# Optimization experiments

Measured on AMD Instinct MI355X. Metric: run time of the kernel, lower is better.

The kernel has to match this reference:

```python
import jax, jax.numpy as jnp
import numpy as np

SHAPES = [(64, 64), (32, 32), (16, 16), (8, 8)]  # (H,W) per level, strides 8..64 of a 512px image
D, NH, NLV, NP, NLAYERS, DFF = 256, 8, 4, 4, 6, 1024
HD = D // NH
B = 4


def setup_inputs() -> dict:
    key = jax.random.key(0)
    ks = jax.random.split(key, 32)
    inp = {}
    for l, (h, w) in enumerate(SHAPES):
        inp[f"src{l}"] = jax.random.normal(ks[l], (B, D, h, w), jnp.float32)
        inp[f"pos{l}"] = jax.random.normal(ks[4 + l], (B, D, h, w), jnp.float32)
    s = 0.02
    p = lambda k, shape: jax.random.normal(k, shape, jnp.float32) * s
    inp["level_embed"] = p(ks[8], (NLV, D))
    inp["W_so"] = p(ks[9], (NLAYERS, D, NH * NLV * NP * 2)); inp["b_so"] = p(ks[10], (NLAYERS, NH * NLV * NP * 2))
    inp["W_aw"] = p(ks[11], (NLAYERS, D, NH * NLV * NP)); inp["b_aw"] = p(ks[12], (NLAYERS, NH * NLV * NP))
    inp["W_v"] = p(ks[13], (NLAYERS, D, D)); inp["b_v"] = p(ks[14], (NLAYERS, D))
    inp["W_o"] = p(ks[15], (NLAYERS, D, D)); inp["b_o"] = p(ks[16], (NLAYERS, D))
    inp["g1"] = jnp.ones((NLAYERS, D)); inp["be1"] = jnp.zeros((NLAYERS, D))
    inp["W_f1"] = p(ks[17], (NLAYERS, D, DFF)); inp["b_f1"] = p(ks[18], (NLAYERS, DFF))
    inp["W_f2"] = p(ks[19], (NLAYERS, DFF, D)); inp["b_f2"] = p(ks[20], (NLAYERS, D))
    inp["g2"] = jnp.ones((NLAYERS, D)); inp["be2"] = jnp.zeros((NLAYERS, D))
    return inp


def _layernorm(x, g, b):
    m = x.mean(-1, keepdims=True)
    v = x.var(-1, keepdims=True)
    return (x - m) * jax.lax.rsqrt(v + 1e-5) * g + b


def _reference_points():
    refs = []
    for (H_, W_) in SHAPES:
        ry = (jnp.arange(H_, dtype=jnp.float32) + 0.5) / H_
        rx = (jnp.arange(W_, dtype=jnp.float32) + 0.5) / W_
        gy, gx = jnp.meshgrid(ry, rx, indexing="ij")
        refs.append(jnp.stack([gx.ravel(), gy.ravel()], -1))
    return jnp.concatenate(refs, 0)  # [S,2] (x,y); valid_ratios==1 so same per level


def _ms_deform_sample(value, loc, aw):
    # value [B,S,NH,HD]; loc [B,S,NH,NLV,NP,2] (x,y in [0,1]); aw [B,S,NH,NLV,NP]
    Bq, S = value.shape[:2]
    v = value.transpose(0, 2, 1, 3)  # [B,NH,S,HD]
    out = jnp.zeros((Bq, NH, S, HD), value.dtype)
    start = 0
    for l, (H_, W_) in enumerate(SHAPES):
        n = H_ * W_
        vl = v[:, :, start:start + n, :]  # [B,NH,H_*W_,HD]
        start += n
        # grid_sample(align_corners=False) semantics: pixel = loc*size - 0.5, zero padding
        x = loc[:, :, :, l, :, 0] * W_ - 0.5  # [B,S,NH,NP]
        y = loc[:, :, :, l, :, 1] * H_ - 0.5
        x0 = jnp.floor(x); y0 = jnp.floor(y)
        wx1 = x - x0; wy1 = y - y0
        acc = jnp.zeros((Bq, NH, S * NP, HD), value.dtype)
        corners = ((0, 0, (1 - wx1) * (1 - wy1)), (1, 0, wx1 * (1 - wy1)),
                   (0, 1, (1 - wx1) * wy1), (1, 1, wx1 * wy1))
        for dx, dy, wgt in corners:
            xi = x0 + dx; yi = y0 + dy
            valid = (xi >= 0) & (xi < W_) & (yi >= 0) & (yi < H_)
            idx = (jnp.clip(yi, 0, H_ - 1) * W_ + jnp.clip(xi, 0, W_ - 1)).astype(jnp.int32)
            idx = idx.transpose(0, 2, 1, 3).reshape(Bq, NH, S * NP)
            w = (wgt * valid).transpose(0, 2, 1, 3).reshape(Bq, NH, S * NP)
            g = jnp.take_along_axis(vl, idx[..., None], axis=2)  # [B,NH,S*NP,HD]
            acc = acc + w[..., None] * g
        acc = acc.reshape(Bq, NH, S, NP, HD)
        awl = aw[:, :, :, l, :].transpose(0, 2, 1, 3)  # [B,NH,S,NP]
        out = out + (acc * awl[..., None]).sum(3)
    return out.transpose(0, 2, 1, 3).reshape(Bq, S, D)


def reference(src0, src1, src2, src3, pos0, pos1, pos2, pos3, level_embed,
              W_so, b_so, W_aw, b_aw, W_v, b_v, W_o, b_o, g1, be1,
              W_f1, b_f1, W_f2, b_f2, g2, be2):
    srcs = [src0, src1, src2, src3]
    poss = [pos0, pos1, pos2, pos3]
    src_flat, pos_flat = [], []
    for l in range(NLV):
        src_flat.append(srcs[l].reshape(B, D, -1).transpose(0, 2, 1))
        pos_flat.append(poss[l].reshape(B, D, -1).transpose(0, 2, 1) + level_embed[l])
    src = jnp.concatenate(src_flat, 1)   # [B,S,D]
    pos = jnp.concatenate(pos_flat, 1)
    S = src.shape[1]
    ref = _reference_points()  # [S,2]
    normalizer = jnp.array([[w, h] for (h, w) in SHAPES], jnp.float32)  # [NLV,2] = (W,H)

    out = src
    for i in range(NLAYERS):
        q = out + pos
        off = (q @ W_so[i] + b_so[i]).reshape(B, S, NH, NLV, NP, 2)
        loc = ref[None, :, None, None, None, :] + off / normalizer[None, None, None, :, None, :]
        aw = jax.nn.softmax((q @ W_aw[i] + b_aw[i]).reshape(B, S, NH, NLV * NP), -1)
        aw = aw.reshape(B, S, NH, NLV, NP)
        val = (out @ W_v[i] + b_v[i]).reshape(B, S, NH, HD)
        att = _ms_deform_sample(val, loc, aw) @ W_o[i] + b_o[i]
        x = _layernorm(out + att, g1[i], be1[i])
        ffn = jax.nn.relu(x @ W_f1[i] + b_f1[i]) @ W_f2[i] + b_f2[i]
        out = _layernorm(x + ffn, g2[i], be2[i])

    spatial_shapes = jnp.array(SHAPES, jnp.int32)
    level_start_index = jnp.concatenate([jnp.zeros((1,), jnp.int32),
                                         jnp.cumsum(spatial_shapes.prod(1))[:-1]])
    return out, spatial_shapes, level_start_index
```

## Files before the change

### kernel.cpp

```cpp
#include <hip/hip_runtime.h>
#include <cstdint>

#define SSn 5440
#define TTn 21760
#define TD ((size_t)TTn*256)
#define NL 6

typedef short bf16x8 __attribute__((ext_vector_type(8)));
typedef float f32x4 __attribute__((ext_vector_type(4)));
typedef float f32x2 __attribute__((ext_vector_type(2)));
typedef unsigned short u16x4 __attribute__((ext_vector_type(4)));
typedef unsigned short ushort_t;

__device__ __forceinline__ ushort_t f2b(float f) {
  uint32_t x = __float_as_uint(f);
  uint32_t r = x + 0x7FFFu + ((x >> 16) & 1u);
  return (ushort_t)(r >> 16);
}
__device__ __forceinline__ float b2f(ushort_t u) {
  return __uint_as_float((uint32_t)u << 16);
}

__global__ __launch_bounds__(256) void prep_kernel(
    const float* __restrict__ s0, const float* __restrict__ p0,
    const float* __restrict__ s1, const float* __restrict__ p1,
    const float* __restrict__ s2, const float* __restrict__ p2,
    const float* __restrict__ s3, const float* __restrict__ p3,
    const float* __restrict__ lev,
    float* __restrict__ cur, ushort_t* __restrict__ cur_b,
    ushort_t* __restrict__ pos_b, ushort_t* __restrict__ q_b)
{
  __shared__ float ts[64][65];
  __shared__ float tp[64][65];
  int bx = blockIdx.x;
  int b = bx / 340, r = bx % 340;
  const float *sp, *pp; int l, HW, start, dt, ptile;
  if (r < 256)      { l=0; HW=4096; start=0;    sp=s0; pp=p0; dt=r>>6;       ptile=r&63; }
  else if (r < 320) { l=1; HW=1024; start=4096; sp=s1; pp=p1; dt=(r-256)>>4; ptile=(r-256)&15; }
  else if (r < 336) { l=2; HW=256;  start=5120; sp=s2; pp=p2; dt=(r-320)>>2; ptile=(r-320)&3; }
  else              { l=3; HW=64;   start=5376; sp=s3; pp=p3; dt=r-336;      ptile=0; }
  int d0 = dt * 64, pp0 = ptile * 64;
  int t = threadIdx.x;
  int rr = t >> 2, c4 = (t & 3) * 16;
  size_t ibase = ((size_t)b * 256 + d0 + rr) * HW + pp0;
  #pragma unroll
  for (int i = 0; i < 4; ++i) {
    f32x4 v = *(const f32x4*)(sp + ibase + c4 + i * 4);
    f32x4 w = *(const f32x4*)(pp + ibase + c4 + i * 4);
    #pragma unroll
    for (int j = 0; j < 4; ++j) { ts[c4 + i*4 + j][rr] = v[j]; tp[c4 + i*4 + j][rr] = w[j]; }
  }
  __syncthreads();
  int token = start + pp0 + rr;
  size_t obase = ((size_t)b * SSn + token) * 256 + d0;
  #pragma unroll
  for (int i = 0; i < 4; ++i) {
    f32x4 cv; u16x4 cb, pb, qb;
    #pragma unroll
    for (int j = 0; j < 4; ++j) {
      float c = ts[rr][c4 + i*4 + j];
      float p = tp[rr][c4 + i*4 + j] + lev[l * 256 + d0 + c4 + i*4 + j];
      cv[j] = c; cb[j] = f2b(c); pb[j] = f2b(p); qb[j] = f2b(c + p);
    }
    *(f32x4*)(cur + obase + c4 + i*4) = cv;
    *(u16x4*)(cur_b + obase + c4 + i*4) = cb;
    *(u16x4*)(pos_b + obase + c4 + i*4) = pb;
    *(u16x4*)(q_b + obase + c4 + i*4) = qb;
  }
}

__global__ __launch_bounds__(256) void wprep_kernel(
    const float* __restrict__ W_so, const float* __restrict__ W_aw,
    const float* __restrict__ W_v,  const float* __restrict__ W_o,
    const float* __restrict__ W_f1, const float* __restrict__ W_f2,
    ushort_t* __restrict__ wt)
{
  __shared__ float tile[64][65];
  int bx = blockIdx.x;
  int layer = bx / 184, r = bx % 184;
  int type, ti;
  if (r < 16)       { type = 0; ti = r; }
  else if (r < 24)  { type = 1; ti = r - 16; }
  else if (r < 40)  { type = 2; ti = r - 24; }
  else if (r < 56)  { type = 3; ti = r - 40; }
  else if (r < 120) { type = 4; ti = r - 56; }
  else              { type = 5; ti = r - 120; }
  const float* src;
  int K, N, dof;
  switch (type) {
    case 0: src = W_so + (size_t)layer * 65536;  K = 256;  N = 256;  dof = 0;      break;
    case 1: src = W_aw + (size_t)layer * 32768;  K = 256;  N = 128;  dof = 65536;  break;
    case 2: src = W_v  + (size_t)layer * 65536;  K = 256;  N = 256;  dof = 98304;  break;
    case 3: src = W_o  + (size_t)layer * 65536;  K = 256;  N = 256;  dof = 163840; break;
    case 4: src = W_f1 + (size_t)layer * 262144; K = 256;  N = 1024; dof = 229376; break;
    default:src = W_f2 + (size_t)layer * 262144; K = 1024; N = 256;  dof = 491520; break;
  }
  int Kt = K >> 6;
  int k0 = (ti % Kt) * 64, n0 = (ti / Kt) * 64;
  ushort_t* dst = wt + (size_t)layer * 753664 + dof;
  int t = threadIdx.x;
  int rr = t >> 2, c4 = (t & 3) * 16;
  #pragma unroll
  for (int i = 0; i < 4; ++i) {
    f32x4 v = *(const f32x4*)(src + (size_t)(k0 + rr) * N + n0 + c4 + i * 4);
    tile[c4 + i*4 + 0][rr] = v[0];
    tile[c4 + i*4 + 1][rr] = v[1];
    tile[c4 + i*4 + 2][rr] = v[2];
    tile[c4 + i*4 + 3][rr] = v[3];
  }
  __syncthreads();
  int vrow = ((rr & 3) << 4) | (rr >> 2);
  #pragma unroll
  for (int i = 0; i < 4; ++i) {
    u16x4 o;
    #pragma unroll
    for (int j = 0; j < 4; ++j) o[j] = f2b(tile[rr][c4 + i*4 + j]);
    *(u16x4*)(dst + (size_t)(n0 + vrow) * K + k0 + c4 + i * 4) = o;
  }
}

__global__ void bias_fuse(const float* __restrict__ bso,
                          const float* __restrict__ baw,
                          float* __restrict__ bsa)
{
  int l = blockIdx.x, t = threadIdx.x;
  bsa[l * 384 + t] = (t < 256) ? bso[l * 256 + t] : baw[l * 128 + t - 256];
}

__device__ __forceinline__ void gemm_body8(
    ushort_t* As, ushort_t* Bs,
    const ushort_t* __restrict__ A, const ushort_t* __restrict__ Bt,
    const float* __restrict__ bias, ushort_t* __restrict__ Cb,
    int N, int n0, int m0, int K, int relu)
{
  int t = threadIdx.x;
  int l = t & 63, w = t >> 6;
  int wr = w >> 1, wc = w & 1;
  int lq = l >> 4, l15 = l & 15, r7 = l & 7;
  f32x4 acc[4][4] = {};

  for (int k0 = 0; k0 < K; k0 += 64) {
    #pragma unroll
    for (int i = 0; i < 4; ++i) {
      int c = i * 512 + t;
      int row = c >> 3;
      int sc = (c & 7) ^ (row & 7);
      __builtin_amdgcn_global_load_lds(
          (const uint32_t*)(A + (size_t)(m0 + row) * K + k0 + sc * 8),
          (uint32_t*)((char*)As + c * 16), 16, 0, 0);
    }
    #pragma unroll
    for (int i = 0; i < 2; ++i) {
      int c = i * 512 + t;
      int row = c >> 3;
      int sc = (c & 7) ^ (row & 7);
      __builtin_amdgcn_global_load_lds(
          (const uint32_t*)(Bt + (size_t)(n0 + row) * K + k0 + sc * 8),
          (uint32_t*)((char*)Bs + c * 16), 16, 0, 0);
    }
    __syncthreads();
    #pragma unroll
    for (int ks = 0; ks < 2; ++ks) {
      bf16x8 af[4], bfr[4];
      int chs = ((ks << 2) + lq) ^ r7;
      #pragma unroll
      for (int mt = 0; mt < 4; ++mt)
        af[mt] = *(const bf16x8*)((const char*)As +
                   (wr * 64 + mt * 16 + l15) * 128 + (chs << 4));
      #pragma unroll
      for (int nt = 0; nt < 4; ++nt)
        bfr[nt] = *(const bf16x8*)((const char*)Bs +
                   (wc * 64 + nt * 16 + l15) * 128 + (chs << 4));
      #pragma unroll
      for (int mt = 0; mt < 4; ++mt)
        #pragma unroll
        for (int nt = 0; nt < 4; ++nt)
          acc[mt][nt] = __builtin_amdgcn_mfma_f32_16x16x32_bf16(
              af[mt], bfr[nt], acc[mt][nt], 0, 0, 0);
    }
    __syncthreads();
  }

  int crow0 = m0 + wr * 64;
  int cb = n0 + wc * 64 + l15 * 4;
  f32x4 bv4 = *(const f32x4*)(bias + cb);
  #pragma unroll
  for (int mt = 0; mt < 4; ++mt) {
    #pragma unroll
    for (int r = 0; r < 4; ++r) {
      int rowg = crow0 + mt * 16 + lq * 4 + r;
      u16x4 o;
      #pragma unroll
      for (int nt = 0; nt < 4; ++nt) {
        float v = acc[mt][nt][r] + bv4[nt];
        if (relu) v = fmaxf(v, 0.f);
        o[nt] = f2b(v);
      }
      *(u16x4*)(Cb + (size_t)rowg * N + cb) = o;
    }
  }
}

__global__ __launch_bounds__(512) void gemm_mfma(
    const ushort_t* __restrict__ A, const ushort_t* __restrict__ Bt,
    const float* __restrict__ bias, ushort_t* __restrict__ Cb,
    int N, int K, int relu)
{
  __shared__ alignas(16) ushort_t As[16384];
  __shared__ alignas(16) ushort_t Bs[8192];
  gemm_body8(As, Bs, A, Bt, bias, Cb, N, blockIdx.y * 128, blockIdx.x * 256, K, relu);
}

__global__ __launch_bounds__(512) void gemm_dual(
    const ushort_t* __restrict__ A0, const ushort_t* __restrict__ Bt0,
    const float* __restrict__ bias0, ushort_t* __restrict__ C0,
    const ushort_t* __restrict__ A1, const ushort_t* __restrict__ Bt1,
    const float* __restrict__ bias1, ushort_t* __restrict__ C1,
    int K)
{
  __shared__ alignas(16) ushort_t As[16384];
  __shared__ alignas(16) ushort_t Bs[8192];
  int gy = blockIdx.y;
  if (gy < 3)
    gemm_body8(As, Bs, A0, Bt0, bias0, C0, 384, gy * 128, blockIdx.x * 256, K, 0);
  else
    gemm_body8(As, Bs, A1, Bt1, bias1, C1, 256, (gy - 3) * 128, blockIdx.x * 256, K, 0);
}

__global__ __launch_bounds__(512) void gemm_ln(
    const ushort_t* __restrict__ A, const ushort_t* __restrict__ Bt,
    const float* __restrict__ bias, const float* __restrict__ res,
    const float* __restrict__ g, const float* __restrict__ be,
    float* __restrict__ Of, ushort_t* __restrict__ Ob,
    ushort_t* __restrict__ Oq, const ushort_t* __restrict__ posb,
    int K)
{
  __shared__ alignas(16) ushort_t As[64 * 64];
  __shared__ alignas(16) ushort_t Bs[256 * 64];
  __shared__ float psum[64][4];
  __shared__ float psum2[64][4];
  __shared__ float2 mstd[64];
  int t = threadIdx.x;
  int l = t & 63, w = t >> 6;
  int wr = w >> 2, wc = w & 3;
  int m0 = blockIdx.x * 64;
  int lq = l >> 4, l15 = l & 15, r7 = l & 7;
  f32x4 acc[2][4] = {};

  for (int k0 = 0; k0 < K; k0 += 64) {
    {
      int c = t;
      int row = c >> 3;
      int sc = (c & 7) ^ (row & 7);
      __builtin_amdgcn_global_load_lds(
          (const uint32_t*)(A + (size_t)(m0 + row) * K + k0 + sc * 8),
          (uint32_t*)((char*)As + c * 16), 16, 0, 0);
    }
    #pragma unroll
    for (int i = 0; i < 4; ++i) {
      int c = i * 512 + t;
      int row = c >> 3;
      int sc = (c & 7) ^ (row & 7);
      __builtin_amdgcn_global_load_lds(
          (const uint32_t*)(Bt + (size_t)row * K + k0 + sc * 8),
          (uint32_t*)((char*)Bs + c * 16), 16, 0, 0);
    }
    __syncthreads();
    #pragma unroll
    for (int ks = 0; ks < 2; ++ks) {
      bf16x8 af[2], bfr[4];
      int chs = ((ks << 2) + lq) ^ r7;
      #pragma unroll
      for (int mt = 0; mt < 2; ++mt)
        af[mt] = *(const bf16x8*)((const char*)As +
                   (wr * 32 + mt * 16 + l15) * 128 + (chs << 4));
      #pragma unroll
      for (int nt = 0; nt < 4; ++nt)
        bfr[nt] = *(const bf16x8*)((const char*)Bs +
                   (wc * 64 + nt * 16 + l15) * 128 + (chs << 4));
      #pragma unroll
      for (int mt = 0; mt < 2; ++mt)
        #pragma unroll
        for (int nt = 0; nt < 4; ++nt)
          acc[mt][nt] = __builtin_amdgcn_mfma_f32_16x16x32_bf16(
              af[mt], bfr[nt], acc[mt][nt], 0, 0, 0);
    }
    __syncthreads();
  }

  int cb = wc * 64 + l15 * 4;
  f32x4 g4 = *(const f32x4*)(g + cb);
  f32x4 be4 = *(const f32x4*)(be + cb);
  f32x4 b4 = *(const f32x4*)(bias + cb);
  #pragma unroll
  for (int mt = 0; mt < 2; ++mt) {
    #pragma unroll
    for (int r = 0; r < 4; ++r) {
      int rowg = m0 + wr * 32 + mt * 16 + lq * 4 + r;
      f32x4 r4 = *(const f32x4*)(res + (size_t)rowg * 256 + cb);
      #pragma unroll
      for (int nt = 0; nt < 4; ++nt)
        acc[mt][nt][r] += b4[nt] + r4[nt];
    }
  }
  #pragma unroll
  for (int mt = 0; mt < 2; ++mt) {
    #pragma unroll
    for (int r = 0; r < 4; ++r) {
      float s = 0.f, s2 = 0.f;
      #pragma unroll
      for (int nt = 0; nt < 4; ++nt) {
        float v = acc[mt][nt][r];
        s += v; s2 += v * v;
      }
      #pragma unroll
      for (int off = 1; off < 16; off <<= 1) {
        s  += __shfl_xor(s, off);
        s2 += __shfl_xor(s2, off);
      }
      if (l15 == 0) {
        int rloc = wr * 32 + mt * 16 + lq * 4 + r;
        psum[rloc][wc] = s;
        psum2[rloc][wc] = s2;
      }
    }
  }
  __syncthreads();
  if (t < 64) {
    f32x4 a = *(const f32x4*)psum[t];
    f32x4 b = *(const f32x4*)psum2[t];
    float s = a[0] + a[1] + a[2] + a[3];
    float s2 = b[0] + b[1] + b[2] + b[3];
    float mean = s * (1.f / 256.f);
    float var = s2 * (1.f / 256.f) - mean * mean;
    mstd[t] = make_float2(mean, rsqrtf(var + 1e-5f));
  }
  __syncthreads();
  #pragma unroll
  for (int mt = 0; mt < 2; ++mt) {
    #pragma unroll
    for (int r = 0; r < 4; ++r) {
      int rloc = wr * 32 + mt * 16 + lq * 4 + r;
      int rowg = m0 + rloc;
      float2 ms = mstd[rloc];
      size_t o = (size_t)rowg * 256 + cb;
      f32x4 y4; u16x4 yb;
      #pragma unroll
      for (int nt = 0; nt < 4; ++nt) {
        float y = (acc[mt][nt][r] - ms.x) * ms.y * g4[nt] + be4[nt];
        y4[nt] = y; yb[nt] = f2b(y);
      }
      *(f32x4*)(Of + o) = y4;
      *(u16x4*)(Ob + o) = yb;
      if (Oq) {
        u16x4 p4 = *(const u16x4*)(posb + o);
        u16x4 q4;
        #pragma unroll
        for (int nt = 0; nt < 4; ++nt) q4[nt] = f2b(y4[nt] + b2f(p4[nt]));
        *(u16x4*)(Oq + o) = q4;
      }
    }
  }
}

__global__ __launch_bounds__(256, 6) void sample_kernel(
    const ushort_t* __restrict__ val, const ushort_t* __restrict__ sa,
    ushort_t* __restrict__ att)
{
  __shared__ uint4 rec[8][136];
  int tid = threadIdx.x;
  int bid = blockIdx.x;
  int t0 = ((bid & 7) * 340 + (bid >> 3)) * 8;

  #pragma unroll
  for (int it = 0; it < 4; ++it) {
    int idx = it * 256 + tid;
    int tl = idx >> 7;
    int pt = idx & 127;
    int t = t0 + tl;
    int b = t / SSn, s = t % SSn;
    int lvl = (pt >> 2) & 3;
    int st, Wt;
    if (s < 4096)      { st = 0;    Wt = 64; }
    else if (s < 5120) { st = 4096; Wt = 32; }
    else if (s < 5376) { st = 5120; Wt = 16; }
    else               { st = 5376; Wt = 8;  }
    int p = s - st;
    int iy = p / Wt, ix = p % Wt;
    float refx = (ix + 0.5f) / Wt;
    float refy = (iy + 0.5f) / Wt;

    float logit = b2f(sa[(size_t)t * 384 + 256 + pt]);
    float m = logit;
    #pragma unroll
    for (int off = 1; off < 16; off <<= 1) m = fmaxf(m, __shfl_xor(m, off));
    float e = __expf(logit - m);
    float sum = e;
    #pragma unroll
    for (int off = 1; off < 16; off <<= 1) sum += __shfl_xor(sum, off);
    float wa = e / sum;

    const int LWt[4] = {64, 32, 16, 8};
    const int LST[4] = {0, 4096, 5120, 5376};
    int Wl = LWt[lvl], Hl = Wl, stl = LST[lvl];

    uint32_t oxy = *(const uint32_t*)(sa + (size_t)t * 384 + pt * 2);
    float ox = __uint_as_float(oxy << 16);
    float oy = __uint_as_float(oxy & 0xFFFF0000u);
    float x = refx * Wl + ox - 0.5f;
    float y = refy * Hl + oy - 0.5f;
    float x0f = floorf(x), y0f = floorf(y);
    int x0 = (int)x0f, y0 = (int)y0f;
    float wx1 = x - x0f, wy1 = y - y0f;
    int vbase = b * SSn + stl;
    uint32_t ipk[4]; uint32_t wpk[4];
    #pragma unroll
    for (int c = 0; c < 4; ++c) {
      int dx = c & 1, dy = c >> 1;
      int xi = x0 + dx, yi = y0 + dy;
      float wgt = (dx ? wx1 : 1.f - wx1) * (dy ? wy1 : 1.f - wy1);
      bool valid = (xi >= 0) & (xi < Wl) & (yi >= 0) & (yi < Hl);
      int xc = min(max(xi, 0), Wl - 1), yc = min(max(yi, 0), Hl - 1);
      ipk[c] = (uint32_t)(vbase + yc * Wl + xc);
      wpk[c] = valid ? (uint32_t)f2b(wgt * wa) : 0u;
    }
    uint4 r;
    r.x = ipk[0] | (ipk[1] << 16);
    r.y = ipk[2] | (ipk[3] << 16);
    r.z = wpk[0] | (wpk[1] << 16);
    r.w = wpk[2] | (wpk[3] << 16);
    rec[tl][pt + (pt >> 4)] = r;
  }
  __syncthreads();

  int tl = tid >> 5, v = tid & 31;
  int t = t0 + tl;
  int h = v >> 2, j = v & 3;
  int c0 = h * 32 + j * 8;
  uint32_t cb2 = (uint32_t)(c0 * 2);
  const char* vb = (const char*)val;
  f32x2 acA[4] = {}, acB[4] = {};
  #pragma unroll
  for (int k = 0; k < 16; k += 2) {
    uint4 rA = rec[tl][h * 17 + k];
    uint4 rB = rec[tl][h * 17 + k + 1];
    uint32_t oA0 = ((rA.x & 0xFFFFu) << 9) + cb2;
    uint32_t oA1 = ((rA.x >> 16)     << 9) + cb2;
    uint32_t oA2 = ((rA.y & 0xFFFFu) << 9) + cb2;
    uint32_t oA3 = ((rA.y >> 16)     << 9) + cb2;
    uint32_t oB0 = ((rB.x & 0xFFFFu) << 9) + cb2;
    uint32_t oB1 = ((rB.x >> 16)     << 9) + cb2;
    uint32_t oB2 = ((rB.y & 0xFFFFu) << 9) + cb2;
    uint32_t oB3 = ((rB.y >> 16)     << 9) + cb2;
    uint4 uA0 = *(const uint4*)(vb + oA0);
    uint4 uA1 = *(const uint4*)(vb + oA1);
    uint4 uA2 = *(const uint4*)(vb + oA2);
    uint4 uA3 = *(const uint4*)(vb + oA3);
    uint4 uB0 = *(const uint4*)(vb + oB0);
    uint4 uB1 = *(const uint4*)(vb + oB1);
    uint4 uB2 = *(const uint4*)(vb + oB2);
    uint4 uB3 = *(const uint4*)(vb + oB3);
    float wA[4] = { __uint_as_float(rA.z << 16),
                    __uint_as_float(rA.z & 0xFFFF0000u),
                    __uint_as_float(rA.w << 16),
                    __uint_as_float(rA.w & 0xFFFF0000u) };
    float wB[4] = { __uint_as_float(rB.z << 16),
                    __uint_as_float(rB.z & 0xFFFF0000u),
                    __uint_as_float(rB.w << 16),
                    __uint_as_float(rB.w & 0xFFFF0000u) };
    const uint4* uvA[4] = { &uA0, &uA1, &uA2, &uA3 };
    const uint4* uvB[4] = { &uB0, &uB1, &uB2, &uB3 };
    #pragma unroll
    for (int c = 0; c < 4; ++c) {
      uint4 uv = *uvA[c];
      f32x2 w2 = {wA[c], wA[c]};
      f32x2 p0 = {__uint_as_float(uv.x << 16), __uint_as_float(uv.x & 0xFFFF0000u)};
      f32x2 p1 = {__uint_as_float(uv.y << 16), __uint_as_float(uv.y & 0xFFFF0000u)};
      f32x2 p2 = {__uint_as_float(uv.z << 16), __uint_as_float(uv.z & 0xFFFF0000u)};
      f32x2 p3 = {__uint_as_float(uv.w << 16), __uint_as_float(uv.w & 0xFFFF0000u)};
      acA[0] += w2 * p0; acA[1] += w2 * p1; acA[2] += w2 * p2; acA[3] += w2 * p3;
    }
    #pragma unroll
    for (int c = 0; c < 4; ++c) {
      uint4 uv = *uvB[c];
      f32x2 w2 = {wB[c], wB[c]};
      f32x2 p0 = {__uint_as_float(uv.x << 16), __uint_as_float(uv.x & 0xFFFF0000u)};
      f32x2 p1 = {__uint_as_float(uv.y << 16), __uint_as_float(uv.y & 0xFFFF0000u)};
      f32x2 p2 = {__uint_as_float(uv.z << 16), __uint_as_float(uv.z & 0xFFFF0000u)};
      f32x2 p3 = {__uint_as_float(uv.w << 16), __uint_as_float(uv.w & 0xFFFF0000u)};
      acB[0] += w2 * p0; acB[1] += w2 * p1; acB[2] += w2 * p2; acB[3] += w2 * p3;
    }
  }
  #pragma unroll
  for (int i = 0; i < 4; ++i) acA[i] += acB[i];
  uint4 pk;
  pk.x = (uint32_t)f2b(acA[0][0]) | ((uint32_t)f2b(acA[0][1]) << 16);
  pk.y = (uint32_t)f2b(acA[1][0]) | ((uint32_t)f2b(acA[1][1]) << 16);
  pk.z = (uint32_t)f2b(acA[2][0]) | ((uint32_t)f2b(acA[2][1]) << 16);
  pk.w = (uint32_t)f2b(acA[3][0]) | ((uint32_t)f2b(acA[3][1]) << 16);
  *(uint4*)(att + (size_t)t * 256 + c0) = pk;
}

__global__ void tail_kernel(float* __restrict__ o) {
  const float v[12] = {64.f, 64.f, 32.f, 32.f, 16.f, 16.f, 8.f, 8.f,
                       0.f, 4096.f, 5120.f, 5376.f};
  int i = threadIdx.x;
  if (i < 12) o[i] = v[i];
}

extern "C" void kernel_launch(void* const* d_in, const int* in_sizes, int n_in,
                              void* d_out, int out_size, void* d_ws, size_t ws_size,
                              hipStream_t stream)
{
  const float* s0  = (const float*)d_in[0];
  const float* p0  = (const float*)d_in[1];
  const float* s1  = (const float*)d_in[2];
  const float* p1  = (const float*)d_in[3];
  const float* s2  = (const float*)d_in[4];
  const float* p2  = (const float*)d_in[5];
  const float* s3  = (const float*)d_in[6];
  const float* p3  = (const float*)d_in[7];
  const float* lev = (const float*)d_in[8];
  const float* W_so = (const float*)d_in[9];
  const float* b_so = (const float*)d_in[10];
  const float* W_aw = (const float*)d_in[11];
  const float* b_aw = (const float*)d_in[12];
  const float* W_v  = (const float*)d_in[13];
  const float* b_v  = (const float*)d_in[14];
  const float* W_o  = (const float*)d_in[15];
  const float* b_o  = (const float*)d_in[16];
  const float* g1   = (const float*)d_in[17];
  const float* be1  = (const float*)d_in[18];
  const float* W_f1 = (const float*)d_in[19];
  const float* b_f1 = (const float*)d_in[20];
  const float* W_f2 = (const float*)d_in[21];
  const float* b_f2 = (const float*)d_in[22];
  const float* g2   = (const float*)d_in[23];
  const float* be2  = (const float*)d_in[24];

  float* out = (float*)d_out;
  float* ws  = (float*)d_ws;

  ushort_t* pos_b = (ushort_t*)ws;
  float*    x_f   = ws + TD / 2;
  ushort_t* q_b   = (ushort_t*)(ws + TD / 2 + TD);
  ushort_t* cur_b = (ushort_t*)(ws + 2 * TD);
  ushort_t* x_b   = (ushort_t*)(ws + 2 * TD + TD / 2);
  ushort_t* sa_b  = (ushort_t*)(ws + 3 * TD);
  ushort_t* val_b = (ushort_t*)(ws + 3 * TD + 3 * (TD / 4));
  ushort_t* h_b   = (ushort_t*)(ws + 3 * TD);
  ushort_t* wt    = (ushort_t*)(ws + 5 * TD);
  float*    bsa   = ws + 5 * TD + 2260992;

  const size_t LW = 753664;

  wprep_kernel<<<1104, 256, 0, stream>>>(W_so, W_aw, W_v, W_o, W_f1, W_f2, wt);
  bias_fuse<<<NL, 384, 0, stream>>>(b_so, b_aw, bsa);
  prep_kernel<<<1360, 256, 0, stream>>>(s0, p0, s1, p1, s2, p2, s3, p3, lev,
                                        out, cur_b, pos_b, q_b);

  for (int i = 0; i < NL; ++i) {
    ushort_t* wl = wt + (size_t)i * LW;
    const float* bv  = b_v  + (size_t)i * 256;
    const float* bo  = b_o  + (size_t)i * 256;
    const float* bf1 = b_f1 + (size_t)i * 1024;
    const float* bf2 = b_f2 + (size_t)i * 256;

    gemm_dual<<<dim3(85, 5), 512, 0, stream>>>(q_b, wl + 0, bsa + i * 384, sa_b,
                                               cur_b, wl + 98304, bv, val_b, 256);
    sample_kernel<<<TTn / 8, 256, 0, stream>>>(val_b, sa_b, q_b);
    gemm_ln<<<340, 512, 0, stream>>>(q_b, wl + 163840, bo, out,
                                     g1 + i * 256, be1 + i * 256,
                                     x_f, x_b, nullptr, nullptr, 256);
    gemm_mfma<<<dim3(85, 8), 512, 0, stream>>>(x_b, wl + 229376, bf1,
                                               h_b, 1024, 256, 1);
    gemm_ln<<<340, 512, 0, stream>>>(h_b, wl + 491520, bf2, x_f,
                                     g2 + i * 256, be2 + i * 256,
                                     out, cur_b, q_b, pos_b, 1024);
  }

  tail_kernel<<<1, 16, 0, stream>>>(out + TD);
}
```

Baseline: 731.0 us.

## Fuse FFN up-projection, ReLU, down-projection and LayerNorm into one kernel

Replaces the separate FFN1 GEMM and the FFN2+LayerNorm GEMM with one kernel. Each 64-token block keeps its input tile in LDS, computes the hidden activations in 64-wide chunks and accumulates the down-projection in registers. This removes the global write and reread of the 1024-wide hidden tensor and one launch per layer. The cost is that weight tiles are read straight from global memory by every block without LDS staging, occupancy is lower at 256 threads, and the weight prep and bias layouts change to match the new MFMA operand order.

```diff
diff --git a/kernel.cpp b/kernel.cpp
--- a/kernel.cpp
+++ b/kernel.cpp
@@ -109,13 +109,25 @@
     tile[c4 + i*4 + 3][rr] = v[3];
   }
   __syncthreads();
-  int vrow = ((rr & 3) << 4) | (rr >> 2);
-  #pragma unroll
-  for (int i = 0; i < 4; ++i) {
-    u16x4 o;
-    #pragma unroll
-    for (int j = 0; j < 4; ++j) o[j] = f2b(tile[rr][c4 + i*4 + j]);
-    *(u16x4*)(dst + (size_t)(n0 + vrow) * K + k0 + c4 + i * 4) = o;
+  if (type == 5) {
+    #pragma unroll
+    for (int i = 0; i < 4; ++i) {
+      #pragma unroll
+      for (int j = 0; j < 4; ++j) {
+        int kl = c4 + i*4 + j;
+        int kv = ((kl & 3) << 4) | (kl >> 2);
+        dst[(size_t)(n0 + rr) * K + k0 + kv] = f2b(tile[rr][kl]);
+      }
+    }
+  } else {
+    int vrow = ((rr & 3) << 4) | (rr >> 2);
+    #pragma unroll
+    for (int i = 0; i < 4; ++i) {
+      u16x4 o;
+      #pragma unroll
+      for (int j = 0; j < 4; ++j) o[j] = f2b(tile[rr][c4 + i*4 + j]);
+      *(u16x4*)(dst + (size_t)(n0 + vrow) * K + k0 + c4 + i * 4) = o;
+    }
   }
 }
 
@@ -125,6 +137,14 @@
 {
   int l = blockIdx.x, t = threadIdx.x;
   bsa[l * 384 + t] = (t < 256) ? bso[l * 256 + t] : baw[l * 128 + t - 256];
+}
+
+__global__ void bias_fuse2(const float* __restrict__ bf1,
+                           float* __restrict__ bf1v)
+{
+  int l = blockIdx.x, v = threadIdx.x;
+  int orig = (v & ~63) | (4 * (v & 15) + ((v >> 4) & 3));
+  bf1v[l * 1024 + v] = bf1[l * 1024 + orig];
 }
 
 __device__ __forceinline__ void gemm_body8(
@@ -201,16 +221,6 @@
   }
 }
 
-__global__ __launch_bounds__(512) void gemm_mfma(
-    const ushort_t* __restrict__ A, const ushort_t* __restrict__ Bt,
-    const float* __restrict__ bias, ushort_t* __restrict__ Cb,
-    int N, int K, int relu)
-{
-  __shared__ alignas(16) ushort_t As[16384];
-  __shared__ alignas(16) ushort_t Bs[8192];
-  gemm_body8(As, Bs, A, Bt, bias, Cb, N, blockIdx.y * 128, blockIdx.x * 256, K, relu);
-}
-
 __global__ __launch_bounds__(512) void gemm_dual(
     const ushort_t* __restrict__ A0, const ushort_t* __restrict__ Bt0,
     const float* __restrict__ bias0, ushort_t* __restrict__ C0,
@@ -232,7 +242,6 @@
     const float* __restrict__ bias, const float* __restrict__ res,
     const float* __restrict__ g, const float* __restrict__ be,
     float* __restrict__ Of, ushort_t* __restrict__ Ob,
-    ushort_t* __restrict__ Oq, const ushort_t* __restrict__ posb,
     int K)
 {
   __shared__ alignas(16) ushort_t As[64 * 64];
@@ -352,13 +361,150 @@
       }
       *(f32x4*)(Of + o) = y4;
       *(u16x4*)(Ob + o) = yb;
-      if (Oq) {
-        u16x4 p4 = *(const u16x4*)(posb + o);
-        u16x4 q4;
+    }
+  }
+}
+
+__global__ __launch_bounds__(256) void ffn_fused(
+    const ushort_t* __restrict__ xb, const float* __restrict__ xf,
+    const ushort_t* __restrict__ W1, const ushort_t* __restrict__ W2,
+    const float* __restrict__ b1v, const float* __restrict__ b2,
+    const float* __restrict__ g, const float* __restrict__ be,
+    float* __restrict__ Of, ushort_t* __restrict__ Ob,
+    ushort_t* __restrict__ Oq, const ushort_t* __restrict__ posb)
+{
+  __shared__ alignas(16) ushort_t Xs[64 * 256];
+  __shared__ alignas(16) ushort_t Hs[64 * 64];
+  __shared__ float psum[64][4];
+  __shared__ float psum2[64][4];
+  __shared__ float2 mstd[64];
+  int t = threadIdx.x;
+  int l = t & 63, w = t >> 6;
+  int lq = l >> 4, l15 = l & 15;
+  int m0 = blockIdx.x * 64;
+
+  #pragma unroll
+  for (int i = 0; i < 8; ++i) {
+    int c = i * 256 + t;
+    int row = c >> 5, cw = c & 31;
+    int sc = (cw & 24) | ((cw & 7) ^ (row & 7));
+    __builtin_amdgcn_global_load_lds(
+        (const uint32_t*)(xb + (size_t)(m0 + row) * 256 + sc * 8),
+        (uint32_t*)((char*)Xs + c * 16), 16, 0, 0);
+  }
+  __syncthreads();
+
+  f32x4 acc2[4][4] = {};
+  #pragma unroll 1
+  for (int c = 0; c < 16; ++c) {
+    f32x4 acc1[4] = {};
+    #pragma unroll
+    for (int ks = 0; ks < 8; ++ks) {
+      bf16x8 a1 = *(const bf16x8*)(W1 +
+          ((size_t)(c * 64 + w * 16 + l15)) * 256 + ks * 32 + lq * 8);
+      #pragma unroll
+      for (int nt = 0; nt < 4; ++nt) {
+        int tk = nt * 16 + l15;
+        int kc = ks * 4 + lq;
+        int swz = (kc & 24) | ((kc & 7) ^ (tk & 7));
+        bf16x8 b = *(const bf16x8*)((const char*)Xs + tk * 512 + (swz << 4));
+        acc1[nt] = __builtin_amdgcn_mfma_f32_16x16x32_bf16(a1, b, acc1[nt], 0, 0, 0);
+      }
+    }
+    __syncthreads();
+    {
+      f32x4 bb = *(const f32x4*)(b1v + c * 64 + w * 16 + lq * 4);
+      int hc = w * 2 + (lq >> 1);
+      #pragma unroll
+      for (int nt = 0; nt < 4; ++nt) {
+        int tk = nt * 16 + l15;
+        u16x4 hv;
         #pragma unroll
-        for (int nt = 0; nt < 4; ++nt) q4[nt] = f2b(y4[nt] + b2f(p4[nt]));
-        *(u16x4*)(Oq + o) = q4;
-      }
+        for (int r = 0; r < 4; ++r) {
+          float v = acc1[nt][r] + bb[r];
+          hv[r] = f2b(fmaxf(v, 0.f));
+        }
+        *(u16x4*)((char*)Hs + tk * 128 + ((hc ^ (tk & 7)) << 4) + ((lq & 1) << 3)) = hv;
+      }
+    }
+    __syncthreads();
+    #pragma unroll
+    for (int ks = 0; ks < 2; ++ks) {
+      bf16x8 a2[4];
+      #pragma unroll
+      for (int mt = 0; mt < 4; ++mt)
+        a2[mt] = *(const bf16x8*)(W2 +
+            (size_t)(w * 64 + mt * 16 + l15) * 1024 + c * 64 + ks * 32 + lq * 8);
+      #pragma unroll
+      for (int nt = 0; nt < 4; ++nt) {
+        int tk = nt * 16 + l15;
+        int kc = ks * 4 + lq;
+        bf16x8 hb = *(const bf16x8*)((const char*)Hs + tk * 128 + ((kc ^ (tk & 7)) << 4));
+        #pragma unroll
+        for (int mt = 0; mt < 4; ++mt)
+          acc2[mt][nt] = __builtin_amdgcn_mfma_f32_16x16x32_bf16(a2[mt], hb, acc2[mt][nt], 0, 0, 0);
+      }
+    }
+  }
+
+  f32x4 b24[4], g4[4], be4[4];
+  #pragma unroll
+  for (int mt = 0; mt < 4; ++mt) {
+    int ch = w * 64 + mt * 16 + lq * 4;
+    b24[mt] = *(const f32x4*)(b2 + ch);
+    g4[mt]  = *(const f32x4*)(g + ch);
+    be4[mt] = *(const f32x4*)(be + ch);
+  }
+  #pragma unroll
+  for (int nt = 0; nt < 4; ++nt) {
+    int tk = nt * 16 + l15;
+    #pragma unroll
+    for (int mt = 0; mt < 4; ++mt) {
+      f32x4 r4 = *(const f32x4*)(xf + (size_t)(m0 + tk) * 256 + w * 64 + mt * 16 + lq * 4);
+      #pragma unroll
+      for (int r = 0; r < 4; ++r)
+        acc2[mt][nt][r] += b24[mt][r] + r4[r];
+    }
+    float s = 0.f, s2 = 0.f;
+    #pragma unroll
+    for (int mt = 0; mt < 4; ++mt)
+      #pragma unroll
+      for (int r = 0; r < 4; ++r) {
+        float v = acc2[mt][nt][r];
+        s += v; s2 += v * v;
+      }
+    s  += __shfl_xor(s, 16);  s  += __shfl_xor(s, 32);
+    s2 += __shfl_xor(s2, 16); s2 += __shfl_xor(s2, 32);
+    if (lq == 0) { psum[tk][w] = s; psum2[tk][w] = s2; }
+  }
+  __syncthreads();
+  if (t < 64) {
+    f32x4 a = *(const f32x4*)psum[t];
+    f32x4 b = *(const f32x4*)psum2[t];
+    float s = a[0] + a[1] + a[2] + a[3];
+    float s2 = b[0] + b[1] + b[2] + b[3];
+    float mean = s * (1.f / 256.f);
+    float var = s2 * (1.f / 256.f) - mean * mean;
+    mstd[t] = make_float2(mean, rsqrtf(var + 1e-5f));
+  }
+  __syncthreads();
+  #pragma unroll
+  for (int nt = 0; nt < 4; ++nt) {
+    int tk = nt * 16 + l15;
+    float2 ms = mstd[tk];
+    #pragma unroll
+    for (int mt = 0; mt < 4; ++mt) {
+      size_t o = (size_t)(m0 + tk) * 256 + w * 64 + mt * 16 + lq * 4;
+      f32x4 y4; u16x4 yb, q4;
+      u16x4 p4 = *(const u16x4*)(posb + o);
+      #pragma unroll
+      for (int r = 0; r < 4; ++r) {
+        float y = (acc2[mt][nt][r] - ms.x) * ms.y * g4[mt][r] + be4[mt][r];
+        y4[r] = y; yb[r] = f2b(y); q4[r] = f2b(y + b2f(p4[r]));
+      }
+      *(f32x4*)(Of + o) = y4;
+      *(u16x4*)(Ob + o) = yb;
+      *(u16x4*)(Oq + o) = q4;
     }
   }
 }
@@ -548,14 +694,15 @@
   ushort_t* x_b   = (ushort_t*)(ws + 2 * TD + TD / 2);
   ushort_t* sa_b  = (ushort_t*)(ws + 3 * TD);
   ushort_t* val_b = (ushort_t*)(ws + 3 * TD + 3 * (TD / 4));
-  ushort_t* h_b   = (ushort_t*)(ws + 3 * TD);
   ushort_t* wt    = (ushort_t*)(ws + 5 * TD);
   float*    bsa   = ws + 5 * TD + 2260992;
+  float*    bf1v  = bsa + 2304;
 
   const size_t LW = 753664;
 
   wprep_kernel<<<1104, 256, 0, stream>>>(W_so, W_aw, W_v, W_o, W_f1, W_f2, wt);
   bias_fuse<<<NL, 384, 0, stream>>>(b_so, b_aw, bsa);
+  bias_fuse2<<<NL, 1024, 0, stream>>>(b_f1, bf1v);
   prep_kernel<<<1360, 256, 0, stream>>>(s0, p0, s1, p1, s2, p2, s3, p3, lev,
                                         out, cur_b, pos_b, q_b);
 
@@ -563,7 +710,6 @@
     ushort_t* wl = wt + (size_t)i * LW;
     const float* bv  = b_v  + (size_t)i * 256;
     const float* bo  = b_o  + (size_t)i * 256;
-    const float* bf1 = b_f1 + (size_t)i * 1024;
     const float* bf2 = b_f2 + (size_t)i * 256;
 
     gemm_dual<<<dim3(85, 5), 512, 0, stream>>>(q_b, wl + 0, bsa + i * 384, sa_b,
@@ -571,12 +717,12 @@
     sample_kernel<<<TTn / 8, 256, 0, stream>>>(val_b, sa_b, q_b);
     gemm_ln<<<340, 512, 0, stream>>>(q_b, wl + 163840, bo, out,
                                      g1 + i * 256, be1 + i * 256,
-                                     x_f, x_b, nullptr, nullptr, 256);
-    gemm_mfma<<<dim3(85, 8), 512, 0, stream>>>(x_b, wl + 229376, bf1,
-                                               h_b, 1024, 256, 1);
-    gemm_ln<<<340, 512, 0, stream>>>(h_b, wl + 491520, bf2, x_f,
-                                     g2 + i * 256, be2 + i * 256,
-                                     out, cur_b, q_b, pos_b, 1024);
+                                     x_f, x_b, 256);
+    ffn_fused<<<340, 256, 0, stream>>>(x_b, x_f,
+                                       wl + 229376, wl + 491520,
+                                       bf1v + i * 1024, bf2,
+                                       g2 + i * 256, be2 + i * 256,
+                                       out, cur_b, q_b, pos_b);
   }
 
   tail_kernel<<<1, 16, 0, stream>>>(out + TD);
```

Result: slower. 890.3 us (+21.8%).
